# Kernel tuning notes

Measured on AMD Instinct MI355X. Metric: run time of the kernel, lower is better.

The kernel has to match this reference:

```python
import jax, jax.numpy as jnp
import numpy as np

B, D_IN, H, L, K, E, NL = 16384, 768, 1024, 128, 8192, 128, 3
CC = 0.25  # commitment cost
sg = jax.lax.stop_gradient


def _ln(x, g, b):
    # torch nn.LayerNorm, eps=1e-5
    m = jnp.mean(x, -1, keepdims=True)
    v = jnp.mean((x - m) ** 2, -1, keepdims=True)
    return (x - m) / jnp.sqrt(v + 1e-5) * g + b


def setup_inputs() -> dict:
    key = jax.random.key(0)
    ks = iter(jax.random.split(key, 32))
    def n(sh, s=0.02):
        return jax.random.normal(next(ks), sh, jnp.float32) * s
    return dict(
        x=jax.random.normal(next(ks), (B, D_IN), jnp.float32),
        eps=jax.random.normal(next(ks), (B, L), jnp.float32),
        enc_w1=n((D_IN, H)), enc_b1=jnp.zeros((H,), jnp.float32),
        enc_w2=n((H, H)), enc_b2=jnp.zeros((H,), jnp.float32),
        enc_w3=n((H, H)), enc_b3=jnp.zeros((H,), jnp.float32),
        mu_w=n((H, L)), mu_b=jnp.zeros((L,), jnp.float32),
        var_w=n((H, L)), var_b=jnp.zeros((L,), jnp.float32),
        dec_w1=n((L, H)), dec_b1=jnp.zeros((H,), jnp.float32),
        dec_w2=n((H, H)), dec_b2=jnp.zeros((H,), jnp.float32),
        dec_w3=n((H, D_IN)), dec_b3=jnp.zeros((D_IN,), jnp.float32),
        ln_g=jnp.ones((NL, L), jnp.float32),
        ln_b=jnp.zeros((NL, L), jnp.float32),
        q_in_w=n((NL, L, E)), q_in_b=jnp.zeros((NL, E), jnp.float32),
        codebook=jax.random.uniform(next(ks), (NL, K, E), jnp.float32,
                                    -1.0 / K, 1.0 / K),
        q_out_w=n((NL, E, L)), q_out_b=jnp.zeros((NL, L), jnp.float32),
    )


def reference(x, eps, enc_w1, enc_b1, enc_w2, enc_b2, enc_w3, enc_b3,
              mu_w, mu_b, var_w, var_b,
              dec_w1, dec_b1, dec_w2, dec_b2, dec_w3, dec_b3,
              ln_g, ln_b, q_in_w, q_in_b, codebook, q_out_w, q_out_b):
    # encoder MLP
    h = jax.nn.relu(x @ enc_w1 + enc_b1)
    h = jax.nn.relu(h @ enc_w2 + enc_b2)
    h = h @ enc_w3 + enc_b3
    mu = h @ mu_w + mu_b
    log_var = h @ var_w + var_b
    z = mu + eps * jnp.exp(0.5 * log_var)  # reparameterize

    # residual quantization over NL layers
    cur = z
    quantized = jnp.zeros_like(z)
    total_loss = jnp.float32(0.0)
    for i in range(NL):  # small fixed layer count
        nr = _ln(cur, ln_g[i], ln_b[i])                  # [B, L]
        f = nr @ q_in_w[i] + q_in_b[i]                   # [B, E]
        cb = codebook[i]                                 # [K, E]
        d = (jnp.sum(f * f, axis=1, keepdims=True)
             + jnp.sum(cb * cb, axis=1)
             - 2.0 * f @ cb.T)                           # [B, K]
        idx = jnp.argmin(d, axis=1)                      # [B]
        q = cb[idx] @ q_out_w[i] + q_out_b[i]            # gather == onehot@cb
        e_loss = jnp.mean((sg(q) - nr) ** 2)
        q_loss = jnp.mean((q - sg(nr)) ** 2)
        total_loss = total_loss + q_loss + CC * e_loss
        q_st = nr + sg(q - nr)                           # straight-through
        quantized = quantized + q_st
        cur = cur - q_st

    # decoder MLP
    r = jax.nn.relu(quantized @ dec_w1 + dec_b1)
    r = jax.nn.relu(r @ dec_w2 + dec_b2)
    recon = r @ dec_w3 + dec_b3
    return recon, mu, log_var, total_loss
```

## Files before the change

### kernel.cpp

```cpp
#include <hip/hip_runtime.h>
#include <stdint.h>


typedef float   floatx4  __attribute__((ext_vector_type(4)));
typedef __bf16  bf16x8   __attribute__((ext_vector_type(8)));
typedef unsigned short ushort4v __attribute__((ext_vector_type(4)));
typedef unsigned short bfbits;

#define AS1 __attribute__((address_space(1)))
#define AS3 __attribute__((address_space(3)))

__device__ __forceinline__ bfbits f2bf(float f) {
  unsigned u = __float_as_uint(f);
  u += 0x7fffu + ((u >> 16) & 1u);
  return (bfbits)(u >> 16);
}

__device__ __forceinline__ void load_lds16(const void* g, void* l) {
  __builtin_amdgcn_global_load_lds((AS1 void*)g, (AS3 void*)l, 16, 0, 0);
}

__global__ __launch_bounds__(256) void cvt_bf16_kernel(
    const float* __restrict__ in, bfbits* __restrict__ out, long n4) {
  long i = (long)blockIdx.x * 256 + threadIdx.x;
  if (i >= n4) return;
  float4 v = ((const float4*)in)[i];
  ushort4v o = { f2bf(v.x), f2bf(v.y), f2bf(v.z), f2bf(v.w) };
  ((ushort4v*)out)[i] = o;
}

__global__ __launch_bounds__(256) void transpose_bf16_kernel(
    const float* __restrict__ W, bfbits* __restrict__ Wt, int K, int N) {
  __shared__ float t[32][33];
  const long base = (long)blockIdx.z * K * N;
  const int k0 = blockIdx.y * 32, n0 = blockIdx.x * 32;
  const int tx = threadIdx.x & 31, ty = threadIdx.x >> 5;
#pragma unroll
  for (int j = 0; j < 32; j += 8)
    t[ty + j][tx] = W[base + (long)(k0 + ty + j) * N + n0 + tx];
  __syncthreads();
#pragma unroll
  for (int j = 0; j < 32; j += 8)
    Wt[base + (long)(n0 + ty + j) * K + k0 + tx] = f2bf(t[tx][ty + j]);
}

__global__ __launch_bounds__(256) void rownorm_kernel(
    const float* __restrict__ cb, float* __restrict__ out) {
  const int wave = threadIdx.x >> 6, lane = threadIdx.x & 63;
  const long row = (long)blockIdx.x * 4 + wave;
  const float* r = cb + row * 128;
  float a = r[lane], b = r[lane + 64];
  float s = a * a + b * b;
#pragma unroll
  for (int off = 1; off < 64; off <<= 1) s += __shfl_xor(s, off);
  if (lane == 0) out[row] = s;
}

template <bool RELU, bool OUTF32, bool DUAL>
__global__ __launch_bounds__(256) void gemm_kernel(
    const bfbits* __restrict__ A, const bfbits* __restrict__ Bt,
    const float* __restrict__ bias, bfbits* __restrict__ Cb,
    float* __restrict__ Cf, float* __restrict__ Cf2, int N, int Kd) {
  __shared__ bfbits Als[128 * 64];
  __shared__ bfbits Bls[128 * 64];
  const int tid = threadIdx.x;
  const int wave = tid >> 6, lane = tid & 63;
  const int wr = wave >> 1, wc = wave & 1;
  const int row0 = blockIdx.x << 7, col0 = blockIdx.y << 7;
  const int l15 = lane & 15, l16 = lane >> 4;
  const int jrow = lane >> 3;
  const int gchunk = (lane & 7) ^ jrow;

  floatx4 acc[4][4] = {};

  for (int k0 = 0; k0 < Kd; k0 += 64) {
    __syncthreads();
#pragma unroll
    for (int j = 0; j < 4; ++j) {
      const int gi = wave * 4 + j;
      const int r = gi * 8 + jrow;
      load_lds16(A + (long)(row0 + r) * Kd + (k0 + gchunk * 8),
                 Als + gi * 512 + lane * 8);
      load_lds16(Bt + (long)(col0 + r) * Kd + (k0 + gchunk * 8),
                 Bls + gi * 512 + lane * 8);
    }
    __syncthreads();
#pragma unroll
    for (int kk = 0; kk < 2; ++kk) {
      bf16x8 af[4], bf[4];
#pragma unroll
      for (int t = 0; t < 4; ++t) {
        const int ar = wr * 64 + t * 16 + l15;
        af[t] = *(const bf16x8*)(Als + ar * 64 + (((kk * 4 + l16) ^ (ar & 7)) * 8));
        const int br = wc * 64 + t * 16 + l15;
        bf[t] = *(const bf16x8*)(Bls + br * 64 + (((kk * 4 + l16) ^ (br & 7)) * 8));
      }
#pragma unroll
      for (int i = 0; i < 4; ++i)
#pragma unroll
        for (int jn = 0; jn < 4; ++jn)
          acc[i][jn] = __builtin_amdgcn_mfma_f32_16x16x32_bf16(
              af[i], bf[jn], acc[i][jn], 0, 0, 0);
    }
  }

#pragma unroll
  for (int mt = 0; mt < 4; ++mt) {
#pragma unroll
    for (int nt = 0; nt < 4; ++nt) {
      const int col = col0 + wc * 64 + nt * 16 + l15;
      const float bv = bias[col];
      const int rowb = row0 + wr * 64 + mt * 16 + l16 * 4;
#pragma unroll
      for (int r = 0; r < 4; ++r) {
        float v = acc[mt][nt][r] + bv;
        if (RELU) v = fmaxf(v, 0.f);
        if (DUAL) {
          if (col < 128) Cf[(long)(rowb + r) * 128 + col] = v;
          else           Cf2[(long)(rowb + r) * 128 + col - 128] = v;
        } else {
          const long idx = (long)(rowb + r) * N + col;
          if (OUTF32) Cf[idx] = v; else Cb[idx] = f2bf(v);
        }
      }
    }
  }
}

template <bool RELU, bool OUTF32>
__global__ __launch_bounds__(512, 2) void gemm256_kernel(
    const bfbits* __restrict__ A, const bfbits* __restrict__ Bt,
    const float* __restrict__ bias, bfbits* __restrict__ Cb,
    float* __restrict__ Cf, int N, int Kd) {
  __shared__ alignas(16) bfbits As[2][256 * 64];
  __shared__ alignas(16) bfbits Bs[2][256 * 64];
  const int tid = threadIdx.x;
  const int w = tid >> 6, lane = tid & 63;
  const int wr = w >> 2, wc = w & 3;
  const int l15 = lane & 15, l16 = lane >> 4;
  const int jrow = lane >> 3;
  const int gch = (lane & 7) ^ jrow;

  const int nbx = gridDim.x, nby = gridDim.y;
  const int nwg = nbx * nby;
  const int cpx = nwg >> 3;
  const int lid = blockIdx.y * nbx + blockIdx.x;
  const int swz = (lid & 7) * cpx + (lid >> 3);
  const int bm = swz / nby, bn = swz % nby;
  const long row0 = (long)bm << 8;
  const long col0 = (long)bn << 8;

  const int NT = Kd >> 6;

  auto stageA = [&](int t, int hh) {
    const bfbits* src = A + (row0 + hh * 128) * Kd + t * 64 + gch * 8;
    bfbits* dst = &As[t & 1][hh * 8192];
#pragma unroll
    for (int q = 0; q < 2; ++q) {
      const int gi = q * 8 + w;
      load_lds16(src + (long)(gi * 8 + jrow) * Kd, dst + gi * 512 + lane * 8);
    }
  };
  auto stageB = [&](int t, int hh) {
    const bfbits* src = Bt + (col0 + hh * 128) * Kd + t * 64 + gch * 8;
    bfbits* dst = &Bs[t & 1][hh * 8192];
#pragma unroll
    for (int q = 0; q < 2; ++q) {
      const int gi = q * 8 + w;
      load_lds16(src + (long)(gi * 8 + jrow) * Kd, dst + gi * 512 + lane * 8);
    }
  };

  auto rdA = [&](int p, int i, int kk) -> bf16x8 {
    const int r = wr * 128 + i * 16 + l15;
    return *(const bf16x8*)(&As[p][r * 64 + (((kk * 4 + l16) ^ (r & 7)) * 8)]);
  };
  auto rdB = [&](int p, int j, int kk) -> bf16x8 {
    const int r = wc * 64 + j * 16 + l15;
    return *(const bf16x8*)(&Bs[p][r * 64 + (((kk * 4 + l16) ^ (r & 7)) * 8)]);
  };

  floatx4 acc[8][4] = {};

  stageA(0, 0); stageA(0, 1); stageB(0, 0); stageB(0, 1);
  stageA(1, 0);
  asm volatile("s_waitcnt vmcnt(2)" ::: "memory");
  __builtin_amdgcn_s_barrier();

  for (int s = 0; s < NT; ++s) {
    const int p = s & 1;
    bf16x8 bfr[4];

    {
      bf16x8 af[4];
#pragma unroll
      for (int t = 0; t < 4; ++t) af[t] = rdA(p, t, 0);
#pragma unroll
      for (int t = 0; t < 4; ++t) bfr[t] = rdB(p, t, 0);
      if (s + 1 < NT) stageA(s + 1, 1);
      __builtin_amdgcn_s_barrier();
      asm volatile("s_waitcnt lgkmcnt(0)" ::: "memory");
      __builtin_amdgcn_sched_barrier(0);
      __builtin_amdgcn_s_setprio(1);
#pragma unroll
      for (int i = 0; i < 4; ++i)
#pragma unroll
        for (int j = 0; j < 4; ++j)
          acc[i][j] = __builtin_amdgcn_mfma_f32_16x16x32_bf16(
              af[i], bfr[j], acc[i][j], 0, 0, 0);
      __builtin_amdgcn_s_setprio(0);
      __builtin_amdgcn_s_barrier();
    }
    {
      bf16x8 af[4];
#pragma unroll
      for (int t = 0; t < 4; ++t) af[t] = rdA(p, 4 + t, 0);
      if (s + 1 < NT) { stageB(s + 1, 0); stageB(s + 1, 1); }
      __builtin_amdgcn_s_barrier();
      asm volatile("s_waitcnt lgkmcnt(0)" ::: "memory");
      __builtin_amdgcn_sched_barrier(0);
      __builtin_amdgcn_s_setprio(1);
#pragma unroll
      for (int i = 0; i < 4; ++i)
#pragma unroll
        for (int j = 0; j < 4; ++j)
          acc[4 + i][j] = __builtin_amdgcn_mfma_f32_16x16x32_bf16(
              af[i], bfr[j], acc[4 + i][j], 0, 0, 0);
      __builtin_amdgcn_s_setprio(0);
      __builtin_amdgcn_s_barrier();
    }
    {
      bf16x8 af[4];
#pragma unroll
      for (int t = 0; t < 4; ++t) af[t] = rdA(p, t, 1);
#pragma unroll
      for (int t = 0; t < 4; ++t) bfr[t] = rdB(p, t, 1);
      __builtin_amdgcn_s_barrier();
      asm volatile("s_waitcnt lgkmcnt(0)" ::: "memory");
      __builtin_amdgcn_sched_barrier(0);
      __builtin_amdgcn_s_setprio(1);
#pragma unroll
      for (int i = 0; i < 4; ++i)
#pragma unroll
        for (int j = 0; j < 4; ++j)
          acc[i][j] = __builtin_amdgcn_mfma_f32_16x16x32_bf16(
              af[i], bfr[j], acc[i][j], 0, 0, 0);
      __builtin_amdgcn_s_setprio(0);
      __builtin_amdgcn_s_barrier();
    }
    {
      bf16x8 af[4];
#pragma unroll
      for (int t = 0; t < 4; ++t) af[t] = rdA(p, 4 + t, 1);
      __builtin_amdgcn_s_barrier();
      asm volatile("s_waitcnt lgkmcnt(0)" ::: "memory");
      __builtin_amdgcn_sched_barrier(0);
      __builtin_amdgcn_s_setprio(1);
#pragma unroll
      for (int i = 0; i < 4; ++i)
#pragma unroll
        for (int j = 0; j < 4; ++j)
          acc[4 + i][j] = __builtin_amdgcn_mfma_f32_16x16x32_bf16(
              af[i], bfr[j], acc[4 + i][j], 0, 0, 0);
      __builtin_amdgcn_s_setprio(0);
      __builtin_amdgcn_s_barrier();
    }
    if (s + 1 < NT) {
      if (s + 2 < NT) {
        stageA(s + 2, 0);
        asm volatile("s_waitcnt vmcnt(2)" ::: "memory");
      } else {
        asm volatile("s_waitcnt vmcnt(0)" ::: "memory");
      }
      __builtin_amdgcn_s_barrier();
    }
  }

#pragma unroll
  for (int i = 0; i < 8; ++i) {
    const long rowb = row0 + wr * 128 + i * 16 + l16 * 4;
#pragma unroll
    for (int j = 0; j < 4; ++j) {
      const int col = (int)col0 + wc * 64 + j * 16 + l15;
      const float bv = bias[col];
#pragma unroll
      for (int r = 0; r < 4; ++r) {
        float v = acc[i][j][r] + bv;
        if (RELU) v = fmaxf(v, 0.f);
        const long idx = (rowb + r) * N + col;
        if (OUTF32) Cf[idx] = v; else Cb[idx] = f2bf(v);
      }
    }
  }
}

template <bool OUTF32>
__global__ __launch_bounds__(256) void gemm_n128_kernel(
    const bfbits* __restrict__ A, const bfbits* __restrict__ Bt,
    const float* __restrict__ bias, bfbits* __restrict__ Cb,
    float* __restrict__ Cf) {
  __shared__ bfbits Als[64 * 64];
  __shared__ bfbits Bls[128 * 64];
  const int tid = threadIdx.x;
  const int wave = tid >> 6, lane = tid & 63;
  const int wr = wave >> 1, wc = wave & 1;
  const int row0 = blockIdx.x << 6;
  const int l15 = lane & 15, l16 = lane >> 4;
  const int jrow = lane >> 3;
  const int gchunk = (lane & 7) ^ jrow;

  floatx4 acc[2][4] = {};

  for (int k0 = 0; k0 < 128; k0 += 64) {
    __syncthreads();
    {
#pragma unroll
      for (int j = 0; j < 2; ++j) {
        const int gi = wave * 2 + j;
        const int r = gi * 8 + jrow;
        load_lds16(A + (long)(row0 + r) * 128 + (k0 + gchunk * 8),
                   Als + gi * 512 + lane * 8);
      }
#pragma unroll
      for (int j = 0; j < 4; ++j) {
        const int gi = wave * 4 + j;
        const int r = gi * 8 + jrow;
        load_lds16(Bt + (long)r * 128 + (k0 + gchunk * 8),
                   Bls + gi * 512 + lane * 8);
      }
    }
    __syncthreads();
#pragma unroll
    for (int kk = 0; kk < 2; ++kk) {
      bf16x8 af[2], bf[4];
#pragma unroll
      for (int t = 0; t < 2; ++t) {
        const int ar = wr * 32 + t * 16 + l15;
        af[t] = *(const bf16x8*)(Als + ar * 64 + (((kk * 4 + l16) ^ (ar & 7)) * 8));
      }
#pragma unroll
      for (int t = 0; t < 4; ++t) {
        const int br = wc * 64 + t * 16 + l15;
        bf[t] = *(const bf16x8*)(Bls + br * 64 + (((kk * 4 + l16) ^ (br & 7)) * 8));
      }
#pragma unroll
      for (int i = 0; i < 2; ++i)
#pragma unroll
        for (int jn = 0; jn < 4; ++jn)
          acc[i][jn] = __builtin_amdgcn_mfma_f32_16x16x32_bf16(
              af[i], bf[jn], acc[i][jn], 0, 0, 0);
    }
  }

#pragma unroll
  for (int mt = 0; mt < 2; ++mt) {
#pragma unroll
    for (int nt = 0; nt < 4; ++nt) {
      const int col = wc * 64 + nt * 16 + l15;
      const float bv = bias[col];
      const int rowb = row0 + wr * 32 + mt * 16 + l16 * 4;
#pragma unroll
      for (int r = 0; r < 4; ++r) {
        const float v = acc[mt][nt][r] + bv;
        const long idx = (long)(rowb + r) * 128 + col;
        if (OUTF32) Cf[idx] = v; else Cb[idx] = f2bf(v);
      }
    }
  }
}

__global__ __launch_bounds__(512, 2) void dist2_kernel(
    const bfbits* __restrict__ A,
    const bfbits* __restrict__ Bt,
    const float* __restrict__ cbnorm,
    float* __restrict__ cand) {
  __shared__ alignas(16) bfbits Bls[2][128 * 128];
  const int tid = threadIdx.x;
  const int wave = tid >> 6, lane = tid & 63;
  const int wr = wave & 3, wc = wave >> 2;
  const int l15 = lane & 15, l16 = lane >> 4;
  const int row0 = blockIdx.y * 256;
  const int col0 = blockIdx.x * 2048;

  bf16x8 af[4][4];
#pragma unroll
  for (int mt = 0; mt < 4; ++mt)
#pragma unroll
    for (int s = 0; s < 4; ++s)
      af[mt][s] = *(const bf16x8*)(A + (long)(row0 + wr * 64 + mt * 16 + l15) * 128 +
                                   s * 32 + l16 * 8);

  auto stage = [&](int t, int p) {
    const bfbits* src = Bt + (long)(col0 + t * 128) * 128;
    bfbits* dst = &Bls[p][0];
#pragma unroll
    for (int q = 0; q < 4; ++q) {
      const int j = q * 512 + tid;
      const int c = j >> 4;
      const int g = (j & 15) ^ (c & 15);
      load_lds16(src + (long)c * 128 + g * 8, dst + (size_t)j * 8);
    }
  };

  stage(0, 0);

  float run_val[4][4];
#pragma unroll
  for (int mt = 0; mt < 4; ++mt)
#pragma unroll
    for (int r = 0; r < 4; ++r) run_val[mt][r] = -3.0e38f;

  __syncthreads();

  for (int t = 0; t < 16; ++t) {
    const bfbits* buf = &Bls[t & 1][0];
    if (t + 1 < 16) stage(t + 1, (t + 1) & 1);

    floatx4 initv[4];
    int gcol[4];
#pragma unroll
    for (int nt = 0; nt < 4; ++nt) {
      const int cl = wc * 64 + nt * 16 + l15;
      const float half_cn = -0.5f * cbnorm[col0 + t * 128 + cl];
      initv[nt] = (floatx4){half_cn, half_cn, half_cn, half_cn};
      gcol[nt] = col0 + t * 128 + cl;
    }

    floatx4 acc[4][4];
    {
      bf16x8 bf[4];
#pragma unroll
      for (int nt = 0; nt < 4; ++nt) {
        const int cl = wc * 64 + nt * 16 + l15;
        bf[nt] = *(const bf16x8*)(buf + (size_t)cl * 128 +
                                  (size_t)((l16 ^ l15)) * 8);
      }
#pragma unroll
      for (int mt = 0; mt < 4; ++mt)
#pragma unroll
        for (int nt = 0; nt < 4; ++nt)
          acc[mt][nt] = __builtin_amdgcn_mfma_f32_16x16x32_bf16(
              af[mt][0], bf[nt], initv[nt], 0, 0, 0);
    }
#pragma unroll
    for (int s = 1; s < 4; ++s) {
      bf16x8 bf[4];
#pragma unroll
      for (int nt = 0; nt < 4; ++nt) {
        const int cl = wc * 64 + nt * 16 + l15;
        bf[nt] = *(const bf16x8*)(buf + (size_t)cl * 128 +
                                  (size_t)(((s * 4 + l16) ^ l15)) * 8);
      }
#pragma unroll
      for (int mt = 0; mt < 4; ++mt)
#pragma unroll
        for (int nt = 0; nt < 4; ++nt)
          acc[mt][nt] = __builtin_amdgcn_mfma_f32_16x16x32_bf16(
              af[mt][s], bf[nt], acc[mt][nt], 0, 0, 0);
    }

#pragma unroll
    for (int mt = 0; mt < 4; ++mt)
#pragma unroll
      for (int nt = 0; nt < 4; ++nt)
#pragma unroll
        for (int r = 0; r < 4; ++r) {
          const unsigned emb =
              (__float_as_uint(acc[mt][nt][r]) & 0xFFFFE000u) |
              (unsigned)gcol[nt];
          run_val[mt][r] = fmaxf(run_val[mt][r], __uint_as_float(emb));
        }

    __syncthreads();
  }

#pragma unroll
  for (int mt = 0; mt < 4; ++mt)
#pragma unroll
    for (int r = 0; r < 4; ++r) {
      float v = run_val[mt][r];
#pragma unroll
      for (int off = 1; off < 16; off <<= 1)
        v = fmaxf(v, __shfl_xor(v, off));
      if (l15 == 0) {
        const int row = row0 + wr * 64 + mt * 16 + l16 * 4 + r;
        cand[(long)row * 8 + blockIdx.x * 2 + wc] = v;
      }
    }
}

__global__ __launch_bounds__(256) void argmin8_kernel(
    const float* __restrict__ cand, const float* __restrict__ cb,
    bfbits* __restrict__ cbg) {
  const int wave = threadIdx.x >> 6, lane = threadIdx.x & 63;
  const long row = (long)blockIdx.x * 4 + wave;
  float v = -3.0e38f;
  if (lane < 8) v = cand[row * 8 + lane];
#pragma unroll
  for (int off = 1; off < 8; off <<= 1)
    v = fmaxf(v, __shfl_xor(v, off));
  v = __shfl(v, 0);
  const int k = (int)(__float_as_uint(v) & 0x1FFFu);
  const float* src = cb + (long)k * 128;
  cbg[row * 128 + lane]      = f2bf(src[lane]);
  cbg[row * 128 + lane + 64] = f2bf(src[lane + 64]);
}

__device__ __forceinline__ void ln_row(float c0, float c1, int lane,
                                       const float* __restrict__ g,
                                       const float* __restrict__ bta,
                                       long row, bfbits* __restrict__ nrb,
                                       float* __restrict__ nrf) {
  float s = c0 + c1, sq = c0 * c0 + c1 * c1;
#pragma unroll
  for (int off = 1; off < 64; off <<= 1) {
    s += __shfl_xor(s, off);
    sq += __shfl_xor(sq, off);
  }
  const float m = s * (1.f / 128.f);
  const float var = fmaxf(sq * (1.f / 128.f) - m * m, 0.f);
  const float rstd = rsqrtf(var + 1e-5f);
  const float y0 = (c0 - m) * rstd * g[lane] + bta[lane];
  const float y1 = (c1 - m) * rstd * g[lane + 64] + bta[lane + 64];
  nrf[row * 128 + lane] = y0;
  nrf[row * 128 + lane + 64] = y1;
  nrb[row * 128 + lane] = f2bf(y0);
  nrb[row * 128 + lane + 64] = f2bf(y1);
}

__global__ __launch_bounds__(256) void reparam_ln_kernel(
    const float* __restrict__ mu, const float* __restrict__ lv,
    const float* __restrict__ eps, float* __restrict__ cur,
    float* __restrict__ qnt, const float* __restrict__ g,
    const float* __restrict__ bta, bfbits* __restrict__ nrb,
    float* __restrict__ nrf) {
  const int wave = threadIdx.x >> 6, lane = threadIdx.x & 63;
  const long row = (long)blockIdx.x * 4 + wave;
  const long i0 = row * 128 + lane, i1 = i0 + 64;
  const float z0 = mu[i0] + eps[i0] * expf(0.5f * lv[i0]);
  const float z1 = mu[i1] + eps[i1] * expf(0.5f * lv[i1]);
  cur[i0] = z0; cur[i1] = z1;
  qnt[i0] = 0.f; qnt[i1] = 0.f;
  ln_row(z0, z1, lane, g, bta, row, nrb, nrf);
}

template <bool DO_LN>
__global__ __launch_bounds__(256) void qupd_ln_kernel(
    const float* __restrict__ q, float* __restrict__ nrf,
    float* __restrict__ cur, float* __restrict__ qnt,
    const float* __restrict__ g, const float* __restrict__ bta,
    bfbits* __restrict__ nrb, float* __restrict__ lossp) {
  const int wave = threadIdx.x >> 6, lane = threadIdx.x & 63;
  const long row = (long)blockIdx.x * 4 + wave;
  const long i0 = row * 128 + lane, i1 = i0 + 64;
  const float q0 = q[i0], q1 = q[i1];
  const float d0 = q0 - nrf[i0], d1 = q1 - nrf[i1];
  qnt[i0] += q0; qnt[i1] += q1;
  float p = d0 * d0 + d1 * d1;
#pragma unroll
  for (int off = 1; off < 64; off <<= 1) p += __shfl_xor(p, off);
  __shared__ float sp[4];
  if (lane == 0) sp[wave] = p;
  __syncthreads();
  if (threadIdx.x == 0) lossp[blockIdx.x] = sp[0] + sp[1] + sp[2] + sp[3];
  if (DO_LN) {
    const float c0 = cur[i0] - q0, c1 = cur[i1] - q1;
    cur[i0] = c0; cur[i1] = c1;
    ln_row(c0, c1, lane, g, bta, row, nrb, nrf);
  }
}

__global__ __launch_bounds__(256) void loss_reduce_kernel(
    const float* __restrict__ lossp, float* __restrict__ out, int n) {
  float s = 0.f;
  for (int i = threadIdx.x; i < n; i += 256) s += lossp[i];
#pragma unroll
  for (int off = 1; off < 64; off <<= 1) s += __shfl_xor(s, off);
  __shared__ float sp[4];
  const int wave = threadIdx.x >> 6, lane = threadIdx.x & 63;
  if (lane == 0) sp[wave] = s;
  __syncthreads();
  if (threadIdx.x == 0)
    *out = (sp[0] + sp[1] + sp[2] + sp[3]) * (1.25f / 2097152.f);
}

static void launch_gemm(bool relu, bool outf32, const bfbits* A,
                        const bfbits* Bt, const float* bias, bfbits* Cb,
                        float* Cf, int M, int N, int Kd, hipStream_t s) {
  dim3 g(M / 128, N / 128), b(256);
  if (relu) {
    gemm_kernel<true, false, false><<<g, b, 0, s>>>(A, Bt, bias, Cb, Cf, nullptr, N, Kd);
  } else if (outf32) {
    gemm_kernel<false, true, false><<<g, b, 0, s>>>(A, Bt, bias, Cb, Cf, nullptr, N, Kd);
  } else {
    gemm_kernel<false, false, false><<<g, b, 0, s>>>(A, Bt, bias, Cb, Cf, nullptr, N, Kd);
  }
}

static void launch_gemm256(bool relu, bool outf32, const bfbits* A,
                           const bfbits* Bt, const float* bias, bfbits* Cb,
                           float* Cf, int M, int N, int Kd, hipStream_t s) {
  dim3 g(M / 256, N / 256), b(512);
  if (relu) {
    gemm256_kernel<true, false><<<g, b, 0, s>>>(A, Bt, bias, Cb, Cf, N, Kd);
  } else if (outf32) {
    gemm256_kernel<false, true><<<g, b, 0, s>>>(A, Bt, bias, Cb, Cf, N, Kd);
  } else {
    gemm256_kernel<false, false><<<g, b, 0, s>>>(A, Bt, bias, Cb, Cf, N, Kd);
  }
}

extern "C" void kernel_launch(void* const* d_in, const int* in_sizes, int n_in,
                              void* d_out, int out_size, void* d_ws,
                              size_t ws_size, hipStream_t stream) {
  (void)in_sizes; (void)n_in; (void)out_size; (void)ws_size;
  constexpr long B = 16384, DIN = 768, H = 1024, L = 128, K = 8192;

  const float* x    = (const float*)d_in[0];
  const float* eps  = (const float*)d_in[1];
  const float* ew1  = (const float*)d_in[2];
  const float* eb1  = (const float*)d_in[3];
  const float* ew2  = (const float*)d_in[4];
  const float* eb2  = (const float*)d_in[5];
  const float* ew3  = (const float*)d_in[6];
  const float* eb3  = (const float*)d_in[7];
  const float* muw  = (const float*)d_in[8];
  const float* mub  = (const float*)d_in[9];
  const float* vaw  = (const float*)d_in[10];
  const float* vab  = (const float*)d_in[11];
  const float* dw1  = (const float*)d_in[12];
  const float* db1  = (const float*)d_in[13];
  const float* dw2  = (const float*)d_in[14];
  const float* db2  = (const float*)d_in[15];
  const float* dw3  = (const float*)d_in[16];
  const float* db3  = (const float*)d_in[17];
  const float* lng  = (const float*)d_in[18];
  const float* lnb  = (const float*)d_in[19];
  const float* qinw = (const float*)d_in[20];
  const float* qinb = (const float*)d_in[21];
  const float* cb   = (const float*)d_in[22];
  const float* qow  = (const float*)d_in[23];
  const float* qob  = (const float*)d_in[24];

  float* out = (float*)d_out;
  float* out_mu   = out + B * DIN;
  float* out_lv   = out_mu + B * L;
  float* out_loss = out_lv + B * L;

  char* ws = (char*)d_ws;
  constexpr size_t O_W1T  = 0;
  constexpr size_t O_W2T  = O_W1T + 1024 * 768 * 2;
  constexpr size_t O_W3T  = O_W2T + 1024 * 1024 * 2;
  constexpr size_t O_MUT  = O_W3T + 1024 * 1024 * 2;
  constexpr size_t O_VART = O_MUT + 128 * 1024 * 2;
  constexpr size_t O_DW1T = O_VART + 128 * 1024 * 2;
  constexpr size_t O_DW2T = O_DW1T + 1024 * 128 * 2;
  constexpr size_t O_DW3T = O_DW2T + 1024 * 1024 * 2;
  constexpr size_t O_QINT = O_DW3T + 768 * 1024 * 2;
  constexpr size_t O_QOUT = O_QINT + 3 * 128 * 128 * 2;
  constexpr size_t O_CBB  = O_QOUT + 3 * 128 * 128 * 2;
  constexpr size_t O_CBN  = O_CBB + 3 * 8192 * 128 * 2;
  constexpr size_t O_B2   = O_CBN + 3 * 8192 * 4;
  constexpr size_t O_LOSSP= O_B2 + 256 * 4;
  constexpr size_t O_CUR  = O_LOSSP + 3 * 4096 * 4;
  constexpr size_t O_QNT  = O_CUR + B * L * 4;
  constexpr size_t O_NRF  = O_QNT + B * L * 4;
  constexpr size_t O_H1   = O_NRF + B * L * 4;
  constexpr size_t O_H2   = O_H1 + B * H * 2;
  constexpr size_t O_H3   = O_H2 + B * H * 2;
  constexpr size_t O_NRB  = O_H2;
  constexpr size_t O_FB   = O_H2 + B * L * 2;
  constexpr size_t O_CBG  = O_H2 + 2 * B * L * 2;
  constexpr size_t O_QBUF = O_H2 + 3 * B * L * 2;
  constexpr size_t O_CAND = O_H2 + 3 * B * L * 2 + B * L * 4;
  constexpr size_t O_XB   = O_H3;
  constexpr size_t O_QZB  = O_H3;

  bfbits* w1t  = (bfbits*)(ws + O_W1T);
  bfbits* w2t  = (bfbits*)(ws + O_W2T);
  bfbits* w3t  = (bfbits*)(ws + O_W3T);
  bfbits* mut  = (bfbits*)(ws + O_MUT);
  bfbits* vart = (bfbits*)(ws + O_VART);
  bfbits* dw1t = (bfbits*)(ws + O_DW1T);
  bfbits* dw2t = (bfbits*)(ws + O_DW2T);
  bfbits* dw3t = (bfbits*)(ws + O_DW3T);
  bfbits* qint = (bfbits*)(ws + O_QINT);
  bfbits* qout = (bfbits*)(ws + O_QOUT);
  bfbits* cbb  = (bfbits*)(ws + O_CBB);
  float*  cbn  = (float*)(ws + O_CBN);
  float*  bias2= (float*)(ws + O_B2);
  float*  lossp= (float*)(ws + O_LOSSP);
  float*  cur  = (float*)(ws + O_CUR);
  float*  qnt  = (float*)(ws + O_QNT);
  float*  nrf  = (float*)(ws + O_NRF);
  bfbits* h1   = (bfbits*)(ws + O_H1);
  bfbits* h2   = (bfbits*)(ws + O_H2);
  bfbits* h3   = (bfbits*)(ws + O_H3);
  bfbits* nrb  = (bfbits*)(ws + O_NRB);
  bfbits* fb   = (bfbits*)(ws + O_FB);
  bfbits* cbg  = (bfbits*)(ws + O_CBG);
  float*  qbuf = (float*)(ws + O_QBUF);
  float*  cand = (float*)(ws + O_CAND);
  bfbits* xb   = (bfbits*)(ws + O_XB);
  bfbits* qzb  = (bfbits*)(ws + O_QZB);
  bfbits* r1   = h1;
  bfbits* r2   = h2;

  cvt_bf16_kernel<<<dim3((B * DIN) / 4 / 256), dim3(256), 0, stream>>>(x, xb, (B * DIN) / 4);
  cvt_bf16_kernel<<<dim3((3 * K * 128) / 4 / 256), dim3(256), 0, stream>>>(cb, cbb, (3 * K * 128) / 4);
  transpose_bf16_kernel<<<dim3(1024 / 32, 768 / 32, 1), dim3(256), 0, stream>>>(ew1, w1t, 768, 1024);
  transpose_bf16_kernel<<<dim3(32, 32, 1), dim3(256), 0, stream>>>(ew2, w2t, 1024, 1024);
  transpose_bf16_kernel<<<dim3(32, 32, 1), dim3(256), 0, stream>>>(ew3, w3t, 1024, 1024);
  transpose_bf16_kernel<<<dim3(128 / 32, 32, 1), dim3(256), 0, stream>>>(muw, mut, 1024, 128);
  transpose_bf16_kernel<<<dim3(128 / 32, 32, 1), dim3(256), 0, stream>>>(vaw, vart, 1024, 128);
  transpose_bf16_kernel<<<dim3(32, 128 / 32, 1), dim3(256), 0, stream>>>(dw1, dw1t, 128, 1024);
  transpose_bf16_kernel<<<dim3(32, 32, 1), dim3(256), 0, stream>>>(dw2, dw2t, 1024, 1024);
  transpose_bf16_kernel<<<dim3(768 / 32, 32, 1), dim3(256), 0, stream>>>(dw3, dw3t, 1024, 768);
  transpose_bf16_kernel<<<dim3(4, 4, 3), dim3(256), 0, stream>>>(qinw, qint, 128, 128);
  transpose_bf16_kernel<<<dim3(4, 4, 3), dim3(256), 0, stream>>>(qow, qout, 128, 128);
  rownorm_kernel<<<dim3(3 * K / 4), dim3(256), 0, stream>>>(cb, cbn);
  hipMemcpyAsync(bias2, mub, 128 * 4, hipMemcpyDeviceToDevice, stream);
  hipMemcpyAsync(bias2 + 128, vab, 128 * 4, hipMemcpyDeviceToDevice, stream);

  launch_gemm256(true, false, xb, w1t, eb1, h1, nullptr, B, 1024, 768, stream);
  launch_gemm256(true, false, h1, w2t, eb2, h2, nullptr, B, 1024, 1024, stream);
  launch_gemm256(false, false, h2, w3t, eb3, h3, nullptr, B, 1024, 1024, stream);
  gemm_kernel<false, true, true><<<dim3(128, 2), dim3(256), 0, stream>>>(
      h3, mut, bias2, nullptr, out_mu, out_lv, 256, 1024);

  reparam_ln_kernel<<<dim3(B / 4), dim3(256), 0, stream>>>(
      out_mu, out_lv, eps, cur, qnt, lng, lnb, nrb, nrf);

  for (int i = 0; i < 3; ++i) {
    gemm_n128_kernel<false><<<dim3(B / 64), dim3(256), 0, stream>>>(
        nrb, qint + (size_t)i * 128 * 128, qinb + i * 128, fb, nullptr);
    dist2_kernel<<<dim3(4, 64), dim3(512), 0, stream>>>(
        fb, cbb + (size_t)i * K * 128, cbn + (size_t)i * K, cand);
    argmin8_kernel<<<dim3(B / 4), dim3(256), 0, stream>>>(
        cand, cb + (size_t)i * K * 128, cbg);
    gemm_n128_kernel<true><<<dim3(B / 64), dim3(256), 0, stream>>>(
        cbg, qout + (size_t)i * 128 * 128, qob + i * 128, nullptr, qbuf);
    if (i < 2) {
      qupd_ln_kernel<true><<<dim3(B / 4), dim3(256), 0, stream>>>(
          qbuf, nrf, cur, qnt, lng + (i + 1) * 128, lnb + (i + 1) * 128,
          nrb, lossp + (size_t)i * 4096);
    } else {
      qupd_ln_kernel<false><<<dim3(B / 4), dim3(256), 0, stream>>>(
          qbuf, nrf, cur, qnt, nullptr, nullptr, nullptr,
          lossp + (size_t)i * 4096);
    }
  }
  loss_reduce_kernel<<<dim3(1), dim3(256), 0, stream>>>(lossp, out_loss, 3 * 4096);

  cvt_bf16_kernel<<<dim3((B * L) / 4 / 256), dim3(256), 0, stream>>>(qnt, qzb, (B * L) / 4);
  launch_gemm(true, false, qzb, dw1t, db1, r1, nullptr, B, 1024, 128, stream);
  launch_gemm256(true, false, r1, dw2t, db2, r2, nullptr, B, 1024, 1024, stream);
  launch_gemm(false, true, r2, dw3t, db3, nullptr, out, B, 768, 1024, stream);
}
```

Baseline: 638.8 us.

## Deepen prefetch pipelines and trim barriers in GEMM and distance kernels

In the main bf16 GEMM, all of tile s+1's B loads are now issued in the first sub-step and tile s+2's B half is prefetched alongside A, with per-sub-step barriers removed so only one barrier per phase remains. The dist2 kernel moves from double to triple buffering of codebook tiles with a two-ahead prefetch, and replaces the per-tile __syncthreads with an explicit vmcnt wait plus barrier. Codebook norms are preloaded into LDS once instead of read from global memory every tile. Together these aim to hide more load latency and cut synchronisation stalls, at the cost of more LDS (which may reduce occupancy in dist2) and some risk of races from the removed barriers.

```diff
diff --git a/kernel.cpp b/kernel.cpp
--- a/kernel.cpp
+++ b/kernel.cpp
@@ -183,8 +183,8 @@
   floatx4 acc[8][4] = {};
 
   stageA(0, 0); stageA(0, 1); stageB(0, 0); stageB(0, 1);
-  stageA(1, 0);
-  asm volatile("s_waitcnt vmcnt(2)" ::: "memory");
+  stageA(1, 0); stageB(1, 0);
+  asm volatile("s_waitcnt vmcnt(4)" ::: "memory");
   __builtin_amdgcn_s_barrier();
 
   for (int s = 0; s < NT; ++s) {
@@ -197,7 +197,7 @@
       for (int t = 0; t < 4; ++t) af[t] = rdA(p, t, 0);
 #pragma unroll
       for (int t = 0; t < 4; ++t) bfr[t] = rdB(p, t, 0);
-      if (s + 1 < NT) stageA(s + 1, 1);
+      if (s + 1 < NT) { stageA(s + 1, 1); stageB(s + 1, 1); }
       __builtin_amdgcn_s_barrier();
       asm volatile("s_waitcnt lgkmcnt(0)" ::: "memory");
       __builtin_amdgcn_sched_barrier(0);
@@ -209,13 +209,11 @@
           acc[i][j] = __builtin_amdgcn_mfma_f32_16x16x32_bf16(
               af[i], bfr[j], acc[i][j], 0, 0, 0);
       __builtin_amdgcn_s_setprio(0);
-      __builtin_amdgcn_s_barrier();
     }
     {
       bf16x8 af[4];
 #pragma unroll
       for (int t = 0; t < 4; ++t) af[t] = rdA(p, 4 + t, 0);
-      if (s + 1 < NT) { stageB(s + 1, 0); stageB(s + 1, 1); }
       __builtin_amdgcn_s_barrier();
       asm volatile("s_waitcnt lgkmcnt(0)" ::: "memory");
       __builtin_amdgcn_sched_barrier(0);
@@ -227,7 +225,6 @@
           acc[4 + i][j] = __builtin_amdgcn_mfma_f32_16x16x32_bf16(
               af[i], bfr[j], acc[4 + i][j], 0, 0, 0);
       __builtin_amdgcn_s_setprio(0);
-      __builtin_amdgcn_s_barrier();
     }
     {
       bf16x8 af[4];
@@ -246,7 +243,6 @@
           acc[i][j] = __builtin_amdgcn_mfma_f32_16x16x32_bf16(
               af[i], bfr[j], acc[i][j], 0, 0, 0);
       __builtin_amdgcn_s_setprio(0);
-      __builtin_amdgcn_s_barrier();
     }
     {
       bf16x8 af[4];
@@ -263,12 +259,12 @@
           acc[4 + i][j] = __builtin_amdgcn_mfma_f32_16x16x32_bf16(
               af[i], bfr[j], acc[4 + i][j], 0, 0, 0);
       __builtin_amdgcn_s_setprio(0);
+    }
+    if (s + 1 < NT) {
       __builtin_amdgcn_s_barrier();
-    }
-    if (s + 1 < NT) {
       if (s + 2 < NT) {
-        stageA(s + 2, 0);
-        asm volatile("s_waitcnt vmcnt(2)" ::: "memory");
+        stageA(s + 2, 0); stageB(s + 2, 0);
+        asm volatile("s_waitcnt vmcnt(4)" ::: "memory");
       } else {
         asm volatile("s_waitcnt vmcnt(0)" ::: "memory");
       }
@@ -374,7 +370,8 @@
     const bfbits* __restrict__ Bt,
     const float* __restrict__ cbnorm,
     float* __restrict__ cand) {
-  __shared__ alignas(16) bfbits Bls[2][128 * 128];
+  __shared__ alignas(16) bfbits Bls[3][128 * 128];
+  __shared__ float cnl[2048];
   const int tid = threadIdx.x;
   const int wave = tid >> 6, lane = tid & 63;
   const int wr = wave & 3, wc = wave >> 2;
@@ -382,6 +379,8 @@
   const int row0 = blockIdx.y * 256;
   const int col0 = blockIdx.x * 2048;
 
+  ((float4*)cnl)[tid] = ((const float4*)(cbnorm + col0))[tid];
+
   bf16x8 af[4][4];
 #pragma unroll
   for (int mt = 0; mt < 4; ++mt)
@@ -403,6 +402,7 @@
   };
 
   stage(0, 0);
+  stage(1, 1);
 
   float run_val[4][4];
 #pragma unroll
@@ -410,19 +410,22 @@
 #pragma unroll
     for (int r = 0; r < 4; ++r) run_val[mt][r] = -3.0e38f;
 
-  __syncthreads();
+  asm volatile("s_waitcnt lgkmcnt(0)" ::: "memory");
+  __builtin_amdgcn_s_barrier();
 
   for (int t = 0; t < 16; ++t) {
-    const bfbits* buf = &Bls[t & 1][0];
-    if (t + 1 < 16) stage(t + 1, (t + 1) & 1);
-
-    floatx4 initv[4];
+    if (t == 15) asm volatile("s_waitcnt vmcnt(0)" ::: "memory");
+    else         asm volatile("s_waitcnt vmcnt(4)" ::: "memory");
+    __builtin_amdgcn_s_barrier();
+    const bfbits* buf = &Bls[t % 3][0];
+    if (t + 2 < 16) stage(t + 2, (t + 2) % 3);
+
+    float cn[4];
     int gcol[4];
 #pragma unroll
     for (int nt = 0; nt < 4; ++nt) {
       const int cl = wc * 64 + nt * 16 + l15;
-      const float half_cn = -0.5f * cbnorm[col0 + t * 128 + cl];
-      initv[nt] = (floatx4){half_cn, half_cn, half_cn, half_cn};
+      cn[nt] = cnl[t * 128 + cl];
       gcol[nt] = col0 + t * 128 + cl;
     }
 
@@ -438,9 +441,11 @@
 #pragma unroll
       for (int mt = 0; mt < 4; ++mt)
 #pragma unroll
-        for (int nt = 0; nt < 4; ++nt)
+        for (int nt = 0; nt < 4; ++nt) {
+          const float hc = -0.5f * cn[nt];
           acc[mt][nt] = __builtin_amdgcn_mfma_f32_16x16x32_bf16(
-              af[mt][0], bf[nt], initv[nt], 0, 0, 0);
+              af[mt][0], bf[nt], (floatx4){hc, hc, hc, hc}, 0, 0, 0);
+        }
     }
 #pragma unroll
     for (int s = 1; s < 4; ++s) {
@@ -470,8 +475,6 @@
               (unsigned)gcol[nt];
           run_val[mt][r] = fmaxf(run_val[mt][r], __uint_as_float(emb));
         }
-
-    __syncthreads();
   }
 
 #pragma unroll
```

Result: no change. 634.3 us (-0.7%).
